# Optimization experiments

Measured on AMD Instinct MI355X. Metric: run time of the kernel, lower is better.

## Reference

```python
import jax, jax.numpy as jnp
import numpy as np
import math

N = 400000          # nodes at finest depth
E = 2000000         # edges = N * avg_degree
B = 8               # batch of octrees
C_IN = 4            # input feature channels (channel_in)
N_EDGE_TYPE = 5
N_NODE_TYPE = 7     # depth - 1
AVG_DEGREE = 5
C_OUT = 32          # channels[depth_out]
TEMB_CH = 512       # channels[depth_stop]


def swish(v):
    return v * jax.nn.sigmoid(v)


def setup_inputs() -> dict:
    key = jax.random.key(0)
    ks = jax.random.split(key, 12)
    x = jax.random.normal(ks[0], (N, C_IN), jnp.float32)
    t = jax.random.uniform(ks[1], (B,), jnp.float32) * 1000.0
    edge_index = jax.random.randint(ks[2], (2, E), 0, N)
    edge_type = jax.random.randint(ks[3], (E,), 0, N_EDGE_TYPE)
    node_type = jax.random.randint(ks[4], (N,), 0, N_NODE_TYPE)
    batch_id = jax.random.randint(ks[5], (N,), 0, B)
    fan = N_EDGE_TYPE * (C_IN + N_NODE_TYPE)  # 55
    W_conv = jax.random.normal(ks[6], (fan, C_OUT), jnp.float32) / np.sqrt(fan)
    W1 = jax.random.normal(ks[7], (TEMB_CH // 4, TEMB_CH), jnp.float32) / np.sqrt(TEMB_CH // 4)
    b1 = jnp.zeros((TEMB_CH,), jnp.float32)
    W2 = jax.random.normal(ks[8], (TEMB_CH, TEMB_CH), jnp.float32) / np.sqrt(TEMB_CH)
    b2 = jnp.zeros((TEMB_CH,), jnp.float32)
    W_temb = jax.random.normal(ks[9], (TEMB_CH, C_OUT), jnp.float32) / np.sqrt(TEMB_CH)
    return dict(x=x, t=t, edge_index=edge_index, edge_type=edge_type,
                node_type=node_type, batch_id=batch_id, W_conv=W_conv,
                W1=W1, b1=b1, W2=W2, b2=b2, W_temb=W_temb)


def time_embedding(t, W1, b1, W2, b2):
    # TimeEmbedding.forward: sinusoidal embedding -> lin1 -> swish -> lin2
    half = TEMB_CH // 8  # n_channels // 8
    freqs = jnp.exp(jnp.arange(half, dtype=jnp.float32) * (-math.log(10000.0) / (half - 1)))
    ang = t[:, None] * freqs[None, :]             # [B, half]
    emb = jnp.concatenate([jnp.sin(ang), jnp.cos(ang)], axis=1)  # [B, 2*half]
    emb = swish(emb @ W1 + b1)
    return emb @ W2 + b2                           # [B, TEMB_CH]


def graph_conv(x, edge_index, edge_type, node_type, W_conv):
    # dual-octree GraphConv: one-hot node type, per-(node, edge_type) gather-scatter, dense mix
    oh = jax.nn.one_hot(node_type, N_NODE_TYPE, dtype=x.dtype)
    xh = jnp.concatenate([x, oh], axis=1)          # [N, C_IN + N_NODE_TYPE]
    row, col = edge_index[0], edge_index[1]
    idx = row * N_EDGE_TYPE + edge_type            # bucket per (dst node, edge type)
    agg = jax.ops.segment_sum(xh[col], idx, num_segments=N * N_EDGE_TYPE)
    agg = agg.reshape(N, N_EDGE_TYPE * xh.shape[1])
    return (agg @ W_conv) / AVG_DEGREE             # [N, C_OUT]


def reference(x, t, edge_index, edge_type, node_type, batch_id, W_conv, W1, b1, W2, b2, W_temb):
    h = graph_conv(x, edge_index, edge_type, node_type, W_conv)   # conv1 on input features
    temb = time_embedding(t, W1, b1, W2, b2)                       # [B, TEMB_CH]
    inj = swish(temb) @ W_temb                                     # project temb to node channels
    return h + inj[batch_id]                                       # per-node temb injection
```

## Files before the change

kernel.cpp:

```cpp
#include <hip/hip_runtime.h>


#define CH      4096
#define CW      2048
#define CWSH    11
#define WSZ     128
#define WSH     7
#define NW      16
#define NBCMAX  512
#define NFPMAX  8192

__global__ __launch_bounds__(256) void histW_kernel(
    const int* __restrict__ ei, int* __restrict__ counts,
    int* __restrict__ fineRep,
    const float* __restrict__ t, const float* __restrict__ W1,
    float* __restrict__ h1acc, float* __restrict__ h2acc,
    float* __restrict__ inj,
    int E, int NBC, int NFp, int NCHP)
{
    int tid = threadIdx.x;
    if ((int)blockIdx.x >= NCHP) {
        int b = blockIdx.x - NCHP;
        __shared__ float emb[128];
        if (tid < 128) {
            const float kStep = 9.210340371976184f / 63.0f;
            int k = tid & 63;
            float ang = t[b] * expf(-(float)k * kStep);
            emb[tid] = (tid < 64) ? sinf(ang) : cosf(ang);
        }
        __syncthreads();
        for (int j = tid; j < 512; j += 256) {
            float a = 0.f;
            for (int k = 0; k < 128; ++k) a += emb[k] * W1[k * 512 + j];
            h1acc[b * 512 + j] = a;
            h2acc[b * 512 + j] = 0.f;
        }
        if (tid < 32) inj[b * 32 + tid] = 0.f;
        return;
    }
    __shared__ int fh[NFPMAX];
    int c = blockIdx.x;
    for (int i = tid; i < NFp; i += 256) fh[i] = 0;
    __syncthreads();
    int s = c * CH, e = min(s + CH, E);
    for (int i = s + tid; i < e; i += 256)
        atomicAdd(&fh[ei[i] >> WSH], 1);
    __syncthreads();
    int* row = counts + (size_t)c * NBC;
    for (int b = tid; b < NBC; b += 256) {
        int sum = 0;
#pragma unroll
        for (int w = 0; w < NW; ++w) sum += fh[b * NW + w];
        row[b] = sum;
    }
    int* rep = fineRep + (size_t)(blockIdx.x & 7) * NFp;
    for (int i = tid; i < NFp; i += 256) {
        int v = fh[i];
        if (v) atomicAdd(&rep[i], v);
    }
}

__global__ __launch_bounds__(256) void scanA_kernel(
    const int* __restrict__ counts, int* __restrict__ bsums,
    const float* __restrict__ h1acc, const float* __restrict__ b1,
    const float* __restrict__ W2, float* __restrict__ h2acc,
    int M, int NBC, int LOGC, int nblkA)
{
    int tid = threadIdx.x;
    if ((int)blockIdx.x >= nblkA) {
        int p = blockIdx.x - nblkA;
        __shared__ float h1s[64];
        if (tid < 64) {
            int bb = tid >> 3, kk = tid & 7;
            int k = p * 8 + kk;
            float v = h1acc[bb * 512 + k] + b1[k];
            h1s[tid] = v / (1.f + expf(-v));
        }
        __syncthreads();
        for (int jj = 0; jj < 2; ++jj) {
            int j = tid + jj * 256;
            float acc[8] = {};
#pragma unroll
            for (int kk = 0; kk < 8; ++kk) {
                float w = W2[(p * 8 + kk) * 512 + j];
#pragma unroll
                for (int bb = 0; bb < 8; ++bb) acc[bb] += h1s[bb * 8 + kk] * w;
            }
#pragma unroll
            for (int bb = 0; bb < 8; ++bb)
                atomicAdd(&h2acc[bb * 512 + j], acc[bb]);
        }
        return;
    }
    __shared__ int s[256];
    int j0 = blockIdx.x * 4096 + tid * 16;
    int maskC = (1 << LOGC) - 1;
    int p = 0;
#pragma unroll
    for (int k = 0; k < 16; ++k) {
        int j = j0 + k;
        if (j < M) {
            int b = j >> LOGC, c = j & maskC;
            p += counts[(size_t)c * NBC + b];
        }
    }
    s[tid] = p; __syncthreads();
    for (int off = 128; off > 0; off >>= 1) {
        if (tid < off) s[tid] += s[tid + off];
        __syncthreads();
    }
    if (tid == 0) bsums[blockIdx.x] = s[0];
}

__global__ __launch_bounds__(1024) void scanBF_kernel(
    int* __restrict__ bsums, int* __restrict__ bstart,
    const int* __restrict__ fineRep, int* __restrict__ fineStart,
    int nblk, int NBC, int NFp, int E)
{
    __shared__ int s[1024];
    __shared__ int fs[1024];
    int tid = threadIdx.x;
    int v = (tid < nblk) ? bsums[tid] : 0;
    s[tid] = v; __syncthreads();
    for (int off = 1; off < 1024; off <<= 1) {
        int u = (tid >= off) ? s[tid - off] : 0;
        __syncthreads();
        s[tid] += u;
        __syncthreads();
    }
    if (tid < nblk) bsums[tid] = s[tid] - v;
    if (tid == 0) bstart[NBC] = E;
    int PTF = (NFp + 1023) >> 10;
    int b0 = tid * PTF;
    int run = 0;
    for (int q = 0; q < PTF; ++q) {
        int i = b0 + q;
        if (i < NFp) {
            int csum = 0;
#pragma unroll
            for (int r = 0; r < 8; ++r) csum += fineRep[(size_t)r * NFp + i];
            run += csum;
        }
    }
    fs[tid] = run; __syncthreads();
    for (int off = 1; off < 1024; off <<= 1) {
        int u = (tid >= off) ? fs[tid - off] : 0;
        __syncthreads();
        fs[tid] += u;
        __syncthreads();
    }
    int tbase = fs[tid] - run;
    for (int q = 0; q < PTF; ++q) {
        int i = b0 + q;
        if (i < NFp) {
            int csum = 0;
#pragma unroll
            for (int r = 0; r < 8; ++r) csum += fineRep[(size_t)r * NFp + i];
            fineStart[i] = tbase;
            tbase += csum;
        }
    }
    if (tid == 0) fineStart[NFp] = E;
}

__global__ __launch_bounds__(256) void scanC_kernel(
    const int* __restrict__ counts, const int* __restrict__ bsums,
    int* __restrict__ base, int* __restrict__ bstart,
    const float* __restrict__ h2acc, const float* __restrict__ b2,
    const float* __restrict__ Wt, float* __restrict__ inj,
    int M, int NBC, int LOGC, int nblkA)
{
    int tid = threadIdx.x;
    if ((int)blockIdx.x >= nblkA) {
        int ks = blockIdx.x - nblkA;
        __shared__ float sws[8][64];
        for (int i = tid; i < 512; i += 256) {
            int b = i >> 6, kk = i & 63;
            int k = ks * 64 + kk;
            float v = h2acc[b * 512 + k] + b2[k];
            sws[b][kk] = v / (1.f + expf(-v));
        }
        __syncthreads();
        int b = tid >> 5, c = tid & 31;
        float acc = 0.f;
        for (int kk = 0; kk < 64; ++kk)
            acc += sws[b][kk] * Wt[(ks * 64 + kk) * 32 + c];
        atomicAdd(&inj[tid], acc);
        return;
    }
    __shared__ int s[256];
    int j0 = blockIdx.x * 4096 + tid * 16;
    int maskC = (1 << LOGC) - 1;
    int v[16]; int p = 0;
#pragma unroll
    for (int k = 0; k < 16; ++k) {
        int j = j0 + k;
        v[k] = 0;
        if (j < M) {
            int b = j >> LOGC, c = j & maskC;
            v[k] = counts[(size_t)c * NBC + b];
        }
        p += v[k];
    }
    s[tid] = p; __syncthreads();
    for (int off = 1; off < 256; off <<= 1) {
        int u = (tid >= off) ? s[tid - off] : 0;
        __syncthreads();
        s[tid] += u;
        __syncthreads();
    }
    int run = bsums[blockIdx.x] + (s[tid] - p);
#pragma unroll
    for (int k = 0; k < 16; ++k) {
        int j = j0 + k;
        if (j < M) {
            base[j] = run;
            if ((j & maskC) == 0) bstart[j >> LOGC] = run;
            run += v[k];
        }
    }
}

__global__ __launch_bounds__(512) void scatter_kernel(
    const int* __restrict__ ei, const int* __restrict__ etype,
    const int* __restrict__ ntype, const int* __restrict__ base,
    uint2* __restrict__ rec, int E, int NBC, int LOGC)
{
    __shared__ int cur[NBCMAX];
    int tid = threadIdx.x;
    int nwg = gridDim.x;
    int q = nwg >> 3, r = nwg & 7;
    int xcd = blockIdx.x & 7, idx = blockIdx.x >> 3;
    int c = (xcd < r) ? xcd * (q + 1) + idx
                      : r * (q + 1) + (xcd - r) * q + idx;
    for (int b = tid; b < NBC; b += 512)
        cur[b] = base[((size_t)b << LOGC) + c];
    __syncthreads();
    int s = c * CH, e = min(s + CH, E);
    for (int i = s + tid; i < e; i += 512) {
        int row = ei[i], col = ei[E + i];
        int T = etype[i], nt = ntype[col];
        int b = row >> CWSH;
        int slot = atomicAdd(&cur[b], 1);
        uint2 rc;
        rc.x = (unsigned)col | ((unsigned)T << 19) | ((unsigned)nt << 22);
        rc.y = (unsigned)(row & (CW - 1));
        rec[slot] = rc;
    }
}

__global__ __launch_bounds__(1024) void repack_kernel(
    const int* __restrict__ bstart, const int* __restrict__ fineStart,
    const uint2* __restrict__ rec, unsigned* __restrict__ rec2)
{
    __shared__ int cur[NW];
    int tid = threadIdx.x;
    int b = blockIdx.x;
    if (tid < NW) cur[tid] = fineStart[b * NW + tid];
    __syncthreads();
    int s = bstart[b], e = bstart[b + 1];
    for (int i = s + tid; i < e; i += 1024) {
        uint2 rc = rec[i];
        int w = (int)(rc.y >> WSH);
        int slot = atomicAdd(&cur[w], 1);
        rec2[slot] = rc.x | ((rc.y & (WSZ - 1)) << 25);
    }
}

__global__ __launch_bounds__(256) void consume_kernel(
    const int* __restrict__ fineStart, const unsigned* __restrict__ rec2,
    const float* __restrict__ x, const float* __restrict__ Wc,
    const int* __restrict__ batch, const float* __restrict__ inj,
    float* __restrict__ out, int N)
{
    __shared__ __align__(16) float tile[WSZ * 57];
    int tid = threadIdx.x;
    int f = blockIdx.x;
    int node0 = f << WSH;

    for (int i = tid; i < WSZ * 57 / 4; i += 256)
        ((float4*)tile)[i] = make_float4(0.f, 0.f, 0.f, 0.f);
    __syncthreads();

    int s = fineStart[f], e = fineStart[f + 1];
    for (int i = s + tid; i < e; i += 256) {
        unsigned u = rec2[i];
        int col  = (int)(u & 0x7FFFFu);
        int T    = (int)((u >> 19) & 7u);
        int nt   = (int)((u >> 22) & 7u);
        int lrow = (int)(u >> 25);
        float4 xv = ((const float4*)x)[col];
        float* tr = tile + lrow * 57 + T * 11;
        atomicAdd(tr + 0, xv.x);
        atomicAdd(tr + 1, xv.y);
        atomicAdd(tr + 2, xv.z);
        atomicAdd(tr + 3, xv.w);
        atomicAdd(tr + 4 + nt, 1.0f);
    }
    __syncthreads();

    int nodes = N - node0; if (nodes > WSZ) nodes = WSZ;
    int nl = tid & (WSZ - 1);
    int hf = __builtin_amdgcn_readfirstlane((int)tid >> 7);
    if (nl < nodes) {
        const float* ar = tile + nl * 57;
        const float4* wb = ((const float4*)Wc) + hf * 4;
        float4 a0 = {0.f,0.f,0.f,0.f}, a1 = a0, a2 = a0, a3 = a0;
#pragma unroll 5
        for (int k = 0; k < 55; ++k) {
            float a = ar[k];
            float4 w0 = wb[k * 8 + 0];
            float4 w1 = wb[k * 8 + 1];
            float4 w2 = wb[k * 8 + 2];
            float4 w3 = wb[k * 8 + 3];
            a0.x += a * w0.x; a0.y += a * w0.y; a0.z += a * w0.z; a0.w += a * w0.w;
            a1.x += a * w1.x; a1.y += a * w1.y; a1.z += a * w1.z; a1.w += a * w1.w;
            a2.x += a * w2.x; a2.y += a * w2.y; a2.z += a * w2.z; a2.w += a * w2.w;
            a3.x += a * w3.x; a3.y += a * w3.y; a3.z += a * w3.z; a3.w += a * w3.w;
        }
        int n = node0 + nl;
        int bb = batch[n];
        const float4* iv = ((const float4*)inj) + bb * 8 + hf * 4;
        float4 i0 = iv[0], i1 = iv[1], i2 = iv[2], i3 = iv[3];
        float4 o0, o1, o2, o3;
        o0.x = i0.x + 0.2f*a0.x; o0.y = i0.y + 0.2f*a0.y;
        o0.z = i0.z + 0.2f*a0.z; o0.w = i0.w + 0.2f*a0.w;
        o1.x = i1.x + 0.2f*a1.x; o1.y = i1.y + 0.2f*a1.y;
        o1.z = i1.z + 0.2f*a1.z; o1.w = i1.w + 0.2f*a1.w;
        o2.x = i2.x + 0.2f*a2.x; o2.y = i2.y + 0.2f*a2.y;
        o2.z = i2.z + 0.2f*a2.z; o2.w = i2.w + 0.2f*a2.w;
        o3.x = i3.x + 0.2f*a3.x; o3.y = i3.y + 0.2f*a3.y;
        o3.z = i3.z + 0.2f*a3.z; o3.w = i3.w + 0.2f*a3.w;
        float4* op = ((float4*)out) + (size_t)n * 8 + hf * 4;
        op[0] = o0; op[1] = o1; op[2] = o2; op[3] = o3;
    }
}

__global__ __launch_bounds__(256) void temb_fused_kernel(
    const float* __restrict__ t,
    const float* __restrict__ W1, const float* __restrict__ b1,
    const float* __restrict__ W2, const float* __restrict__ b2,
    const float* __restrict__ Wt, float* __restrict__ inj)
{
    int b = blockIdx.x;
    int tid = threadIdx.x;
    __shared__ float emb[128];
    __shared__ float s1[512];
    __shared__ float s2[512];
    __shared__ float red[256];
    float tv = t[b];
    if (tid < 128) {
        const float kStep = 9.210340371976184f / 63.0f;
        int k = tid & 63;
        float ang = tv * expf(-(float)k * kStep);
        emb[tid] = (tid < 64) ? sinf(ang) : cosf(ang);
    }
    __syncthreads();
    {
        float a0 = 0.f, a1 = 0.f;
        for (int k = 0; k < 128; ++k) {
            float e = emb[k];
            a0 += e * W1[k * 512 + tid];
            a1 += e * W1[k * 512 + tid + 256];
        }
        float v0 = a0 + b1[tid], v1 = a1 + b1[tid + 256];
        s1[tid]       = v0 / (1.0f + expf(-v0));
        s1[tid + 256] = v1 / (1.0f + expf(-v1));
    }
    __syncthreads();
    {
        float a0 = 0.f, a1 = 0.f;
        for (int k = 0; k < 512; ++k) {
            float e = s1[k];
            a0 += e * W2[k * 512 + tid];
            a1 += e * W2[k * 512 + tid + 256];
        }
        float v0 = a0 + b2[tid], v1 = a1 + b2[tid + 256];
        s2[tid]       = v0 / (1.0f + expf(-v0));
        s2[tid + 256] = v1 / (1.0f + expf(-v1));
    }
    __syncthreads();
    {
        int c = tid & 31, seg = tid >> 5;
        float acc = 0.f;
        int k0 = seg * 64;
        for (int k = k0; k < k0 + 64; ++k)
            acc += s2[k] * Wt[k * 32 + c];
        red[tid] = acc;
        __syncthreads();
        if (tid < 32) {
            float s = 0.f;
#pragma unroll
            for (int g = 0; g < 8; ++g) s += red[g * 32 + tid];
            inj[b * 32 + tid] = s;
        }
    }
}

__global__ __launch_bounds__(256) void init_kernel(
    const int* __restrict__ batch_id, const float* __restrict__ inj,
    float4* __restrict__ out, int N)
{
    int gid = blockIdx.x * 256 + threadIdx.x;
    if (gid >= N * 8) return;
    int n = gid >> 3, q = gid & 7;
    int b = batch_id[n];
    out[gid] = ((const float4*)inj)[b * 8 + q];
}

__global__ __launch_bounds__(256) void edge_direct_kernel(
    const int* __restrict__ ei, const int* __restrict__ etype,
    const int* __restrict__ ntype, const float* __restrict__ x,
    const float* __restrict__ Wc, float* __restrict__ out, int E)
{
    __shared__ float Ws[55 * 32];
    for (int i = threadIdx.x; i < 55 * 32; i += 256) Ws[i] = Wc[i];
    __syncthreads();
    unsigned total = (unsigned)E * 32u;
    unsigned stride = gridDim.x * 256u;
    for (unsigned idx = blockIdx.x * 256u + threadIdx.x; idx < total;
         idx += stride) {
        int e = (int)(idx >> 5);
        int c = (int)(idx & 31);
        int row = ei[e];
        int col = ei[E + e];
        int T = etype[e];
        int nt = ntype[col];
        float4 xv = ((const float4*)x)[col];
        const float* wb = Ws + T * 352;
        float y = xv.x * wb[c] + xv.y * wb[32 + c] + xv.z * wb[64 + c] +
                  xv.w * wb[96 + c] + wb[(4 + nt) * 32 + c];
        atomicAdd(out + (size_t)row * 32 + c, y * 0.2f);
    }
}

extern "C" void kernel_launch(void* const* d_in, const int* in_sizes, int n_in,
                              void* d_out, int out_size, void* d_ws, size_t ws_size,
                              hipStream_t stream) {
    const float* x     = (const float*)d_in[0];
    const float* t     = (const float*)d_in[1];
    const int*   ei    = (const int*)d_in[2];
    const int*   etype = (const int*)d_in[3];
    const int*   ntype = (const int*)d_in[4];
    const int*   batch = (const int*)d_in[5];
    const float* Wc    = (const float*)d_in[6];
    const float* W1    = (const float*)d_in[7];
    const float* b1    = (const float*)d_in[8];
    const float* W2    = (const float*)d_in[9];
    const float* b2    = (const float*)d_in[10];
    const float* Wt    = (const float*)d_in[11];
    float* out = (float*)d_out;

    int E = in_sizes[3];
    int N = in_sizes[4];

    int NBC = (N + CW - 1) >> CWSH;
    int NFp = NBC * NW;
    int NFr = (N + WSZ - 1) >> WSH;
    int NCH = (E + CH - 1) / CH;
    int NCHP = 1, LOGC = 0;
    while (NCHP < NCH) { NCHP <<= 1; ++LOGC; }
    size_t M = (size_t)NBC << LOGC;
    int nblkA = (int)((M + 4095) / 4096);

    float* ws     = (float*)d_ws;
    float* h1acc  = ws;
    float* h2acc  = ws + 4096;
    float* inj    = ws + 8192;
    int*   fineRep = (int*)(ws + 8448);
    int*   counts = fineRep + (size_t)8 * NFp;
    int*   base   = counts + M;
    int*   bsums  = base + M;
    int*   bstart = bsums + 1024;
    int*   fineSt = bstart + NBC + 1;
    size_t recOff = 8448 + (size_t)8 * NFp + 2 * M + 1024 + (NBC + 1) + (NFp + 1);
    recOff = (recOff + 1) & ~(size_t)1;
    uint2*    rec  = (uint2*)(ws + recOff);
    unsigned* rec2 = (unsigned*)(ws + recOff + 2 * (size_t)E);

    size_t needBytes = (recOff + 3 * (size_t)E) * 4;
    bool okay = (NBC <= NBCMAX) && (NFp <= NFPMAX) && (nblkA <= 1024) &&
                (ws_size >= needBytes) && (N <= 524288) &&
                (M < (size_t)1 << 30);

    if (okay) {
        hipMemsetAsync(fineRep, 0, (size_t)8 * NFp * 4, stream);

        histW_kernel<<<NCHP + 8, 256, 0, stream>>>(
            ei, counts, fineRep, t, W1, h1acc, h2acc, inj, E, NBC, NFp, NCHP);
        scanA_kernel<<<nblkA + 64, 256, 0, stream>>>(
            counts, bsums, h1acc, b1, W2, h2acc, (int)M, NBC, LOGC, nblkA);
        scanBF_kernel<<<1, 1024, 0, stream>>>(
            bsums, bstart, fineRep, fineSt, nblkA, NBC, NFp, E);
        scanC_kernel<<<nblkA + 8, 256, 0, stream>>>(
            counts, bsums, base, bstart, h2acc, b2, Wt, inj,
            (int)M, NBC, LOGC, nblkA);
        scatter_kernel<<<NCH, 512, 0, stream>>>(
            ei, etype, ntype, base, rec, E, NBC, LOGC);
        repack_kernel<<<NBC, 1024, 0, stream>>>(bstart, fineSt, rec, rec2);
        consume_kernel<<<NFr, 256, 0, stream>>>(
            fineSt, rec2, x, Wc, batch, inj, out, N);
    } else {
        temb_fused_kernel<<<8, 256, 0, stream>>>(t, W1, b1, W2, b2, Wt, inj);
        init_kernel<<<(N * 8 + 255) / 256, 256, 0, stream>>>(
            batch, inj, (float4*)out, N);
        edge_direct_kernel<<<16384, 256, 0, stream>>>(
            ei, etype, ntype, x, Wc, out, E);
    }
}
```

Before: 261.5 us.

## Gather fp16-packed features, vectorize edge loads, widen consume blocks

The histogram kernel now also converts x to packed half precision, so the consume kernel's random gathers fetch 8 bytes per edge instead of 16. The histogram and scatter kernels load edge indices with int4 vectors. The consume kernel runs 512 threads per block, with each thread computing 8 output channels instead of 16. The half-precision gather reduces input precision, which may change accuracy, and the fast path now requires E to be a multiple of 4.

```diff
diff --git a/kernel.cpp b/kernel.cpp
--- a/kernel.cpp
+++ b/kernel.cpp
@@ -1,4 +1,5 @@
 #include <hip/hip_runtime.h>
+#include <hip/hip_fp16.h>
 
 
 #define CH      4096
@@ -10,13 +11,23 @@
 #define NBCMAX  512
 #define NFPMAX  8192
 
+__device__ __forceinline__ unsigned pack2(float a, float b) {
+    __half2 h = __floats2half2_rn(a, b);
+    union { __half2 h; unsigned u; } cv; cv.h = h; return cv.u;
+}
+__device__ __forceinline__ float2 unpack2(unsigned u) {
+    union { unsigned u; __half2 h; } cv; cv.u = u;
+    return __half22float2(cv.h);
+}
+
 __global__ __launch_bounds__(256) void histW_kernel(
     const int* __restrict__ ei, int* __restrict__ counts,
-    int* __restrict__ fineRep,
+    int* __restrict__ fineRep, const float* __restrict__ x,
+    uint2* __restrict__ xh,
     const float* __restrict__ t, const float* __restrict__ W1,
     float* __restrict__ h1acc, float* __restrict__ h2acc,
     float* __restrict__ inj,
-    int E, int NBC, int NFp, int NCHP)
+    int E, int N, int NBC, int NFp, int NCHP)
 {
     int tid = threadIdx.x;
     if ((int)blockIdx.x >= NCHP) {
@@ -43,7 +54,15 @@
     for (int i = tid; i < NFp; i += 256) fh[i] = 0;
     __syncthreads();
     int s = c * CH, e = min(s + CH, E);
-    for (int i = s + tid; i < e; i += 256)
+    int nfull = (e - s) & ~3;
+    for (int i0 = s + tid * 4; i0 < s + nfull; i0 += 1024) {
+        int4 r4 = *(const int4*)&ei[i0];
+        atomicAdd(&fh[r4.x >> WSH], 1);
+        atomicAdd(&fh[r4.y >> WSH], 1);
+        atomicAdd(&fh[r4.z >> WSH], 1);
+        atomicAdd(&fh[r4.w >> WSH], 1);
+    }
+    for (int i = s + nfull + tid; i < e; i += 256)
         atomicAdd(&fh[ei[i] >> WSH], 1);
     __syncthreads();
     int* row = counts + (size_t)c * NBC;
@@ -57,6 +76,15 @@
     for (int i = tid; i < NFp; i += 256) {
         int v = fh[i];
         if (v) atomicAdd(&rep[i], v);
+    }
+    int per = (N + NCHP - 1) / NCHP;
+    int n0 = c * per, n1 = min(n0 + per, N);
+    for (int n = n0 + tid; n < n1; n += 256) {
+        float4 v = ((const float4*)x)[n];
+        uint2 p;
+        p.x = pack2(v.x, v.y);
+        p.y = pack2(v.z, v.w);
+        xh[n] = p;
     }
 }
 
@@ -237,7 +265,24 @@
         cur[b] = base[((size_t)b << LOGC) + c];
     __syncthreads();
     int s = c * CH, e = min(s + CH, E);
-    for (int i = s + tid; i < e; i += 512) {
+    int nfull = (e - s) & ~3;
+    for (int i0 = s + tid * 4; i0 < s + nfull; i0 += 2048) {
+        int4 r4 = *(const int4*)&ei[i0];
+        int4 c4 = *(const int4*)&ei[E + i0];
+        int4 t4 = *(const int4*)&etype[i0];
+#pragma unroll
+        for (int k = 0; k < 4; ++k) {
+            int row = (&r4.x)[k], col = (&c4.x)[k], T = (&t4.x)[k];
+            int nt = ntype[col];
+            int b = row >> CWSH;
+            int slot = atomicAdd(&cur[b], 1);
+            uint2 rc;
+            rc.x = (unsigned)col | ((unsigned)T << 19) | ((unsigned)nt << 22);
+            rc.y = (unsigned)(row & (CW - 1));
+            rec[slot] = rc;
+        }
+    }
+    for (int i = s + nfull + tid; i < e; i += 512) {
         int row = ei[i], col = ei[E + i];
         int T = etype[i], nt = ntype[col];
         int b = row >> CWSH;
@@ -267,9 +312,9 @@
     }
 }
 
-__global__ __launch_bounds__(256) void consume_kernel(
+__global__ __launch_bounds__(512) void consume_kernel(
     const int* __restrict__ fineStart, const unsigned* __restrict__ rec2,
-    const float* __restrict__ x, const float* __restrict__ Wc,
+    const uint2* __restrict__ xh, const float* __restrict__ Wc,
     const int* __restrict__ batch, const float* __restrict__ inj,
     float* __restrict__ out, int N)
 {
@@ -278,23 +323,25 @@
     int f = blockIdx.x;
     int node0 = f << WSH;
 
-    for (int i = tid; i < WSZ * 57 / 4; i += 256)
+    for (int i = tid; i < WSZ * 57 / 4; i += 512)
         ((float4*)tile)[i] = make_float4(0.f, 0.f, 0.f, 0.f);
     __syncthreads();
 
     int s = fineStart[f], e = fineStart[f + 1];
-    for (int i = s + tid; i < e; i += 256) {
+    for (int i = s + tid; i < e; i += 512) {
         unsigned u = rec2[i];
         int col  = (int)(u & 0x7FFFFu);
         int T    = (int)((u >> 19) & 7u);
         int nt   = (int)((u >> 22) & 7u);
         int lrow = (int)(u >> 25);
-        float4 xv = ((const float4*)x)[col];
+        uint2 p = xh[col];
+        float2 f01 = unpack2(p.x);
+        float2 f23 = unpack2(p.y);
         float* tr = tile + lrow * 57 + T * 11;
-        atomicAdd(tr + 0, xv.x);
-        atomicAdd(tr + 1, xv.y);
-        atomicAdd(tr + 2, xv.z);
-        atomicAdd(tr + 3, xv.w);
+        atomicAdd(tr + 0, f01.x);
+        atomicAdd(tr + 1, f01.y);
+        atomicAdd(tr + 2, f23.x);
+        atomicAdd(tr + 3, f23.y);
         atomicAdd(tr + 4 + nt, 1.0f);
     }
     __syncthreads();
@@ -304,35 +351,27 @@
     int hf = __builtin_amdgcn_readfirstlane((int)tid >> 7);
     if (nl < nodes) {
         const float* ar = tile + nl * 57;
-        const float4* wb = ((const float4*)Wc) + hf * 4;
-        float4 a0 = {0.f,0.f,0.f,0.f}, a1 = a0, a2 = a0, a3 = a0;
+        const float4* wq = (const float4*)Wc;
+        float4 a0 = {0.f,0.f,0.f,0.f}, a1 = a0;
 #pragma unroll 5
         for (int k = 0; k < 55; ++k) {
             float a = ar[k];
-            float4 w0 = wb[k * 8 + 0];
-            float4 w1 = wb[k * 8 + 1];
-            float4 w2 = wb[k * 8 + 2];
-            float4 w3 = wb[k * 8 + 3];
+            float4 w0 = wq[k * 8 + hf * 2];
+            float4 w1 = wq[k * 8 + hf * 2 + 1];
             a0.x += a * w0.x; a0.y += a * w0.y; a0.z += a * w0.z; a0.w += a * w0.w;
             a1.x += a * w1.x; a1.y += a * w1.y; a1.z += a * w1.z; a1.w += a * w1.w;
-            a2.x += a * w2.x; a2.y += a * w2.y; a2.z += a * w2.z; a2.w += a * w2.w;
-            a3.x += a * w3.x; a3.y += a * w3.y; a3.z += a * w3.z; a3.w += a * w3.w;
         }
         int n = node0 + nl;
         int bb = batch[n];
-        const float4* iv = ((const float4*)inj) + bb * 8 + hf * 4;
-        float4 i0 = iv[0], i1 = iv[1], i2 = iv[2], i3 = iv[3];
-        float4 o0, o1, o2, o3;
+        const float4* iv = ((const float4*)inj) + bb * 8 + hf * 2;
+        float4 i0 = iv[0], i1 = iv[1];
+        float4 o0, o1;
         o0.x = i0.x + 0.2f*a0.x; o0.y = i0.y + 0.2f*a0.y;
         o0.z = i0.z + 0.2f*a0.z; o0.w = i0.w + 0.2f*a0.w;
         o1.x = i1.x + 0.2f*a1.x; o1.y = i1.y + 0.2f*a1.y;
         o1.z = i1.z + 0.2f*a1.z; o1.w = i1.w + 0.2f*a1.w;
-        o2.x = i2.x + 0.2f*a2.x; o2.y = i2.y + 0.2f*a2.y;
-        o2.z = i2.z + 0.2f*a2.z; o2.w = i2.w + 0.2f*a2.w;
-        o3.x = i3.x + 0.2f*a3.x; o3.y = i3.y + 0.2f*a3.y;
-        o3.z = i3.z + 0.2f*a3.z; o3.w = i3.w + 0.2f*a3.w;
-        float4* op = ((float4*)out) + (size_t)n * 8 + hf * 4;
-        op[0] = o0; op[1] = o1; op[2] = o2; op[3] = o3;
+        float4* op = ((float4*)out) + (size_t)n * 8 + hf * 2;
+        op[0] = o0; op[1] = o1;
     }
 }
 
@@ -467,13 +506,15 @@
     float* h1acc  = ws;
     float* h2acc  = ws + 4096;
     float* inj    = ws + 8192;
-    int*   fineRep = (int*)(ws + 8448);
+    uint2* xh     = (uint2*)(ws + 8448);
+    int*   fineRep = (int*)(ws + 8448 + 2 * (size_t)N);
     int*   counts = fineRep + (size_t)8 * NFp;
     int*   base   = counts + M;
     int*   bsums  = base + M;
     int*   bstart = bsums + 1024;
     int*   fineSt = bstart + NBC + 1;
-    size_t recOff = 8448 + (size_t)8 * NFp + 2 * M + 1024 + (NBC + 1) + (NFp + 1);
+    size_t recOff = 8448 + 2 * (size_t)N + (size_t)8 * NFp + 2 * M + 1024 +
+                    (NBC + 1) + (NFp + 1);
     recOff = (recOff + 1) & ~(size_t)1;
     uint2*    rec  = (uint2*)(ws + recOff);
     unsigned* rec2 = (unsigned*)(ws + recOff + 2 * (size_t)E);
@@ -481,13 +522,14 @@
     size_t needBytes = (recOff + 3 * (size_t)E) * 4;
     bool okay = (NBC <= NBCMAX) && (NFp <= NFPMAX) && (nblkA <= 1024) &&
                 (ws_size >= needBytes) && (N <= 524288) &&
-                (M < (size_t)1 << 30);
+                ((E & 3) == 0) && (M < (size_t)1 << 30);
 
     if (okay) {
         hipMemsetAsync(fineRep, 0, (size_t)8 * NFp * 4, stream);
 
         histW_kernel<<<NCHP + 8, 256, 0, stream>>>(
-            ei, counts, fineRep, t, W1, h1acc, h2acc, inj, E, NBC, NFp, NCHP);
+            ei, counts, fineRep, x, xh, t, W1, h1acc, h2acc, inj,
+            E, N, NBC, NFp, NCHP);
         scanA_kernel<<<nblkA + 64, 256, 0, stream>>>(
             counts, bsums, h1acc, b1, W2, h2acc, (int)M, NBC, LOGC, nblkA);
         scanBF_kernel<<<1, 1024, 0, stream>>>(
@@ -498,8 +540,8 @@
         scatter_kernel<<<NCH, 512, 0, stream>>>(
             ei, etype, ntype, base, rec, E, NBC, LOGC);
         repack_kernel<<<NBC, 1024, 0, stream>>>(bstart, fineSt, rec, rec2);
-        consume_kernel<<<NFr, 256, 0, stream>>>(
-            fineSt, rec2, x, Wc, batch, inj, out, N);
+        consume_kernel<<<NFr, 512, 0, stream>>>(
+            fineSt, rec2, xh, Wc, batch, inj, out, N);
     } else {
         temb_fused_kernel<<<8, 256, 0, stream>>>(t, W1, b1, W2, b2, Wt, inj);
         init_kernel<<<(N * 8 + 255) / 256, 256, 0, stream>>>(
```

New measurement: 251.6 us. -3.8%, faster.
